# Optimization experiments

Hardware: AMD Instinct MI355X
Metric: run time of the kernel (lower is better)

## Reference

```python
import jax, jax.numpy as jnp
import numpy as np

# Constants from retinanet.settings (repo defaults, undefined in snippet; fixed here)
ALPHA = 0.95
GAMMA = 2.0
DAMPENING = 0.7           # DAMPENING_PARAMETER; gt_map simplified to all-False
MAX_POS_DIST = 30.0       # MAX_ANOT_ANCHOR_POSITION_DISTANCE
MAX_ANG_DIST = 20.0       # MAX_ANOT_ANCHOR_ANGLE_DISTANCE
EPS = 1e-4


def setup_inputs() -> dict:
    key = jax.random.key(0)
    k1, k2, k3, k4, k5 = jax.random.split(key, 5)
    B, N, K, C = 4, 300000, 64, 4
    classifications = jax.random.uniform(k1, (B, N, C), jnp.float32, 0.01, 0.99)
    regressions = jax.random.normal(k2, (B, N, 3), jnp.float32) * 5.0
    anchors = jax.random.uniform(k3, (B, N, 3), jnp.float32) * jnp.array([512.0, 512.0, 180.0])
    ann_xy_a = jax.random.uniform(k4, (B, K, 3), jnp.float32) * jnp.array([512.0, 512.0, 180.0])
    ann_cls = jax.random.randint(k5, (B, K, 1), 0, C).astype(jnp.float32)
    annotations = jnp.concatenate([ann_xy_a, ann_cls], axis=-1)  # [B,K,4]
    return {"classifications": classifications, "regressions": regressions,
            "anchors": anchors, "annotations": annotations}


def _per_image(classification, regression, ann, anchor):
    C = classification.shape[1]
    cls = jnp.clip(classification, EPS, 1.0 - EPS)
    # NxK broadcast distance matrices (the tile/transpose chain in the original)
    dx = jnp.abs(anchor[:, 0, None] - ann[None, :, 0])
    dy = jnp.abs(anchor[:, 1, None] - ann[None, :, 1])
    dalpha = jnp.abs(anchor[:, 2, None] - ann[None, :, 2])
    dxy = jnp.sqrt(dx * dx + dy * dy)                         # [N,K]
    dxy_min = jnp.min(dxy, axis=1)                            # [N]
    dxy_argmin = jnp.argmin(dxy, axis=1)                      # [N]
    a = jnp.take_along_axis(dalpha, dxy_argmin[:, None], axis=1)[:, 0]
    # target assignment
    neg = (dxy_min >= 1.5 * MAX_POS_DIST) | (a >= 1.5 * MAX_ANG_DIST)
    pos = (dxy_min < MAX_POS_DIST) & (a < MAX_ANG_DIST)
    assigned = ann[dxy_argmin]                                # [N,4] gather
    targets = jnp.full(cls.shape, -1.0, cls.dtype)
    targets = jnp.where(neg[:, None], 0.0, targets)
    targets = jnp.where(pos[:, None], 0.0, targets)
    onehot = jax.nn.one_hot(assigned[:, 3].astype(jnp.int32), C, dtype=cls.dtype)
    targets = jnp.where(pos[:, None] & (onehot > 0), 1.0, targets)
    num_pos = jnp.sum(pos).astype(cls.dtype)
    denom = jnp.maximum(num_pos, 1.0)
    # focal-weighted BCE
    alpha_factor = jnp.where(targets == 1.0, ALPHA, 1.0 - ALPHA)
    focal_weight = alpha_factor * jnp.where(targets == 1.0, 1.0 - cls, cls) ** GAMMA
    bce = -(targets * jnp.log(cls) + (1.0 - targets) * jnp.log(1.0 - cls))
    cls_loss = jnp.where(targets != -1.0, focal_weight * bce, 0.0) * DAMPENING
    cls_total = jnp.sum(cls_loss) / denom
    t = assigned[:, :3] - anchor
    diff_xy = jnp.abs(t[:, :2] - regression[:, :2])
    loss_xy = jnp.where(diff_xy <= 1.0 / 9.0, 0.5 * 9.0 * diff_xy ** 2, diff_xy - 0.5 / 9.0) * DAMPENING
    diff_ang = jnp.maximum((jnp.abs(t[:, 2] - regression[:, 2]) - 10.0) / 5.0, 0.0) * DAMPENING
    has_pos = num_pos > 0
    xy_mean = jnp.where(has_pos, jnp.sum(loss_xy * pos[:, None]) / (2.0 * denom), 0.0)
    ang_mean = jnp.where(has_pos, jnp.sum(diff_ang * pos) / denom, 0.0)
    return cls_total, xy_mean, ang_mean


def reference(classifications, regressions, anchors, annotations):
    anchor = anchors[0]  # original uses anchors[0,:,:] for all batch elements
    cls_l, xy_l, ang_l = jax.vmap(lambda c, r, an: _per_image(c, r, an, anchor))(
        classifications, regressions, annotations)
    return jnp.stack([jnp.mean(cls_l), jnp.mean(xy_l), jnp.mean(ang_l)])
```

## Files before the change

### kernel.cpp

```cpp
#include <hip/hip_runtime.h>
#include <cmath>

constexpr int Bk = 4;
constexpr int Nk = 300000;
constexpr int Kk = 64;
constexpr int BLOCK = 256;
constexpr int CHUNK = 4;
constexpr int SUPER = BLOCK * CHUNK;
constexpr int PBI = (Nk + SUPER - 1) / SUPER;
constexpr int NBLK = Bk * PBI;

#define C_ALPHA 0.95f
#define C_NALPHA (1.0f - 0.95f)
#define C_DAMP 0.7f


__global__ __launch_bounds__(BLOCK) void focal_main(
    const float* __restrict__ cls_,
    const float* __restrict__ reg_,
    const float* __restrict__ anc_,
    const float* __restrict__ ann_,
    float4* __restrict__ part)
{
    __shared__ float2 s_xy[Kk];
    __shared__ float  s_an[Kk];
    __shared__ float  s_cl[Kk];

    const int b   = blockIdx.x / PBI;
    const int blk = blockIdx.x - b * PBI;
    const int tid = threadIdx.x;
    const int a0  = blk * SUPER + tid * CHUNK;

    if (tid < Kk) {
        const float4 a4 = reinterpret_cast<const float4*>(ann_)[b * Kk + tid];
        s_xy[tid] = make_float2(a4.x, a4.y);
        s_an[tid] = a4.z;
        s_cl[tid] = a4.w;
    }
    __syncthreads();

    const bool full = (a0 + CHUNK) <= Nk;

    float ax[CHUNK], ay[CHUNK], aa[CHUNK];
    if (full) {
        const float4* a4p = reinterpret_cast<const float4*>(anc_);
        const int fb = 3 * (blk * BLOCK + tid);
        const float4 r0 = a4p[fb + 0];
        const float4 r1 = a4p[fb + 1];
        const float4 r2 = a4p[fb + 2];
        ax[0] = r0.x; ay[0] = r0.y; aa[0] = r0.z;
        ax[1] = r0.w; ay[1] = r1.x; aa[1] = r1.y;
        ax[2] = r1.z; ay[2] = r1.w; aa[2] = r2.x;
        ax[3] = r2.y; ay[3] = r2.z; aa[3] = r2.w;
    } else {
        #pragma unroll
        for (int c = 0; c < CHUNK; ++c) {
            const int n = a0 + c;
            if (n < Nk) {
                ax[c] = anc_[(size_t)n * 3 + 0];
                ay[c] = anc_[(size_t)n * 3 + 1];
                aa[c] = anc_[(size_t)n * 3 + 2];
            } else { ax[c] = 1e9f; ay[c] = 1e9f; aa[c] = 0.f; }
        }
    }

    float4 p4[CHUNK];
    if (full) {
        const float4* c4 = reinterpret_cast<const float4*>(cls_) + (size_t)b * Nk + a0;
        #pragma unroll
        for (int c = 0; c < CHUNK; ++c) p4[c] = c4[c];
    } else {
        #pragma unroll
        for (int c = 0; c < CHUNK; ++c) {
            const int n = a0 + c;
            p4[c] = (n < Nk) ? reinterpret_cast<const float4*>(cls_)[(size_t)b * Nk + n]
                             : make_float4(0.5f, 0.5f, 0.5f, 0.5f);
        }
    }

    float best[CHUNK];
    int   arg[CHUNK];
    #pragma unroll
    for (int c = 0; c < CHUNK; ++c) { best[c] = 3.4e38f; arg[c] = 0; }

    #pragma unroll
    for (int k = 0; k < Kk; ++k) {
        const float2 axy = s_xy[k];
        #pragma unroll
        for (int c = 0; c < CHUNK; ++c) {
            const float dx = ax[c] - axy.x;
            const float dy = ay[c] - axy.y;
            const float d  = fmaf(dy, dy, dx * dx);
            if (d < best[c]) { best[c] = d; arg[c] = k; }
        }
    }

    float cls_sum = 0.f, xy_sum = 0.f, ang_sum = 0.f, posn = 0.f;

    #pragma unroll
    for (int c = 0; c < CHUNK; ++c) {
        const bool  valid = full || (a0 + c < Nk);
        const int   a     = arg[c];
        const float aang  = fabsf(aa[c] - s_an[a]);
        const bool  posm  = valid && (best[c] < 900.0f)   && (aang < 20.0f);
        const bool  negm  = valid && ((best[c] >= 2025.0f) || (aang >= 30.0f));
        posn += posm ? 1.0f : 0.0f;

        const float p[4] = {p4[c].x, p4[c].y, p4[c].z, p4[c].w};
        float base = 0.f;
        #pragma unroll
        for (int cc = 0; cc < 4; ++cc) {
            const float pc = fminf(fmaxf(p[cc], 1e-4f), 1.0f - 1e-4f);
            base = fmaf(pc * pc, -__logf(1.0f - pc), base);
        }
        float s = C_NALPHA * base;
        if (posm) {
            const int cidx = (int)s_cl[a];
            float pc = (cidx < 2) ? (cidx == 0 ? p[0] : p[1])
                                  : (cidx == 2 ? p[2] : p[3]);
            pc = fminf(fmaxf(pc, 1e-4f), 1.0f - 1e-4f);
            s -= C_NALPHA * pc * pc * (-__logf(1.0f - pc));
            const float q = 1.0f - pc;
            s += C_ALPHA * q * q * (-__logf(pc));
        }
        cls_sum += (posm || negm) ? s * C_DAMP : 0.f;

        if (posm) {
            const size_t rb = ((size_t)b * Nk + (a0 + c)) * 3;
            const float rx = reg_[rb + 0];
            const float ry = reg_[rb + 1];
            const float ra = reg_[rb + 2];
            const float tx = s_xy[a].x - ax[c];
            const float ty = s_xy[a].y - ay[c];
            const float ta = s_an[a]   - aa[c];
            const float d0 = fabsf(tx - rx);
            const float d1 = fabsf(ty - ry);
            const float l0 = (d0 <= (1.0f / 9.0f)) ? 4.5f * d0 * d0 : d0 - (0.5f / 9.0f);
            const float l1 = (d1 <= (1.0f / 9.0f)) ? 4.5f * d1 * d1 : d1 - (0.5f / 9.0f);
            xy_sum += (l0 + l1) * C_DAMP;
            ang_sum += fmaxf((fabsf(ta - ra) - 10.0f) / 5.0f, 0.0f) * C_DAMP;
        }
    }

    #pragma unroll
    for (int off = 32; off > 0; off >>= 1) {
        cls_sum += __shfl_down(cls_sum, off, 64);
        xy_sum  += __shfl_down(xy_sum,  off, 64);
        ang_sum += __shfl_down(ang_sum, off, 64);
        posn    += __shfl_down(posn,    off, 64);
    }
    __shared__ float r0s[4], r1s[4], r2s[4], r3s[4];
    const int wave = tid >> 6;
    const int lane = tid & 63;
    if (lane == 0) { r0s[wave] = cls_sum; r1s[wave] = xy_sum; r2s[wave] = ang_sum; r3s[wave] = posn; }
    __syncthreads();
    if (tid == 0) {
        part[blockIdx.x] = make_float4(r0s[0] + r0s[1] + r0s[2] + r0s[3],
                                       r1s[0] + r1s[1] + r1s[2] + r1s[3],
                                       r2s[0] + r2s[1] + r2s[2] + r2s[3],
                                       r3s[0] + r3s[1] + r3s[2] + r3s[3]);
    }
}

__global__ __launch_bounds__(256) void focal_finalize(
    const float4* __restrict__ part, float* __restrict__ out)
{
    const int b    = threadIdx.x >> 6;
    const int lane = threadIdx.x & 63;
    double c = 0.0, x = 0.0, g = 0.0, q = 0.0;
    for (int i = lane; i < PBI; i += 64) {
        const float4 p = part[b * PBI + i];
        c += (double)p.x; x += (double)p.y; g += (double)p.z; q += (double)p.w;
    }
    #pragma unroll
    for (int off = 32; off > 0; off >>= 1) {
        c += __shfl_down(c, off, 64);
        x += __shfl_down(x, off, 64);
        g += __shfl_down(g, off, 64);
        q += __shfl_down(q, off, 64);
    }
    __shared__ double sc[4], sx[4], sg[4], sq[4];
    if (lane == 0) { sc[b] = c; sx[b] = x; sg[b] = g; sq[b] = q; }
    __syncthreads();
    if (threadIdx.x == 0) {
        double cm = 0.0, xm = 0.0, am = 0.0;
        for (int bb = 0; bb < Bk; ++bb) {
            const double np_   = sq[bb];
            const double denom = np_ > 1.0 ? np_ : 1.0;
            cm += sc[bb] / denom;
            if (np_ > 0.0) {
                xm += sx[bb] / (2.0 * denom);
                am += sg[bb] / denom;
            }
        }
        out[0] = (float)(cm / (double)Bk);
        out[1] = (float)(xm / (double)Bk);
        out[2] = (float)(am / (double)Bk);
    }
}

extern "C" void kernel_launch(void* const* d_in, const int* in_sizes, int n_in,
                              void* d_out, int out_size, void* d_ws, size_t ws_size,
                              hipStream_t stream)
{
    const float* cls_ = (const float*)d_in[0];
    const float* reg_ = (const float*)d_in[1];
    const float* anc_ = (const float*)d_in[2];
    const float* ann_ = (const float*)d_in[3];
    float4* part = (float4*)d_ws;

    focal_main<<<dim3(NBLK), dim3(BLOCK), 0, stream>>>(cls_, reg_, anc_, ann_, part);
    focal_finalize<<<dim3(1), dim3(256), 0, stream>>>(part, (float*)d_out);
}
```

Baseline: 102.2 us.

## Pack distance and index into uint min, use packed float math, prefetch regressions

The argmin over 64 annotations now packs the squared distance (low 6 mantissa bits cleared) with the annotation index into one unsigned integer and takes an integer min. This replaces the compare-and-select pair per candidate and lets the distance maths use packed two-wide float vectors. Regression values are now loaded unconditionally as coalesced float4 reads alongside the anchors, instead of as scattered scalar loads only for positive anchors. The trade-off is that truncating the distance can change which annotation wins a near tie and shifts the threshold comparisons slightly, and regression bytes are now read for every anchor.

```diff
diff --git a/kernel.cpp b/kernel.cpp
--- a/kernel.cpp
+++ b/kernel.cpp
@@ -1,5 +1,7 @@
 #include <hip/hip_runtime.h>
 #include <cmath>
+
+typedef float v2f __attribute__((ext_vector_type(2)));
 
 constexpr int Bk = 4;
 constexpr int Nk = 300000;
@@ -42,16 +44,29 @@
     const bool full = (a0 + CHUNK) <= Nk;
 
     float ax[CHUNK], ay[CHUNK], aa[CHUNK];
+    float rx[CHUNK], ry[CHUNK], ra[CHUNK];
+    float4 p4[CHUNK];
     if (full) {
         const float4* a4p = reinterpret_cast<const float4*>(anc_);
         const int fb = 3 * (blk * BLOCK + tid);
-        const float4 r0 = a4p[fb + 0];
-        const float4 r1 = a4p[fb + 1];
-        const float4 r2 = a4p[fb + 2];
-        ax[0] = r0.x; ay[0] = r0.y; aa[0] = r0.z;
-        ax[1] = r0.w; ay[1] = r1.x; aa[1] = r1.y;
-        ax[2] = r1.z; ay[2] = r1.w; aa[2] = r2.x;
-        ax[3] = r2.y; ay[3] = r2.z; aa[3] = r2.w;
+        const float4 A0 = a4p[fb + 0];
+        const float4 A1 = a4p[fb + 1];
+        const float4 A2 = a4p[fb + 2];
+        ax[0] = A0.x; ay[0] = A0.y; aa[0] = A0.z;
+        ax[1] = A0.w; ay[1] = A1.x; aa[1] = A1.y;
+        ax[2] = A1.z; ay[2] = A1.w; aa[2] = A2.x;
+        ax[3] = A2.y; ay[3] = A2.z; aa[3] = A2.w;
+        const float4* r4p = reinterpret_cast<const float4*>(reg_) + (size_t)b * (Nk * 3 / 4);
+        const float4 R0 = r4p[fb + 0];
+        const float4 R1 = r4p[fb + 1];
+        const float4 R2 = r4p[fb + 2];
+        rx[0] = R0.x; ry[0] = R0.y; ra[0] = R0.z;
+        rx[1] = R0.w; ry[1] = R1.x; ra[1] = R1.y;
+        rx[2] = R1.z; ry[2] = R1.w; ra[2] = R2.x;
+        rx[3] = R2.y; ry[3] = R2.z; ra[3] = R2.w;
+        const float4* c4 = reinterpret_cast<const float4*>(cls_) + (size_t)b * Nk + a0;
+        #pragma unroll
+        for (int c = 0; c < CHUNK; ++c) p4[c] = c4[c];
     } else {
         #pragma unroll
         for (int c = 0; c < CHUNK; ++c) {
@@ -60,38 +75,35 @@
                 ax[c] = anc_[(size_t)n * 3 + 0];
                 ay[c] = anc_[(size_t)n * 3 + 1];
                 aa[c] = anc_[(size_t)n * 3 + 2];
-            } else { ax[c] = 1e9f; ay[c] = 1e9f; aa[c] = 0.f; }
-        }
-    }
-
-    float4 p4[CHUNK];
-    if (full) {
-        const float4* c4 = reinterpret_cast<const float4*>(cls_) + (size_t)b * Nk + a0;
-        #pragma unroll
-        for (int c = 0; c < CHUNK; ++c) p4[c] = c4[c];
-    } else {
-        #pragma unroll
-        for (int c = 0; c < CHUNK; ++c) {
-            const int n = a0 + c;
-            p4[c] = (n < Nk) ? reinterpret_cast<const float4*>(cls_)[(size_t)b * Nk + n]
-                             : make_float4(0.5f, 0.5f, 0.5f, 0.5f);
-        }
-    }
-
-    float best[CHUNK];
-    int   arg[CHUNK];
-    #pragma unroll
-    for (int c = 0; c < CHUNK; ++c) { best[c] = 3.4e38f; arg[c] = 0; }
+                const size_t rb = ((size_t)b * Nk + n) * 3;
+                rx[c] = reg_[rb + 0]; ry[c] = reg_[rb + 1]; ra[c] = reg_[rb + 2];
+                p4[c] = reinterpret_cast<const float4*>(cls_)[(size_t)b * Nk + n];
+            } else {
+                ax[c] = 1e9f; ay[c] = 1e9f; aa[c] = 0.f;
+                rx[c] = 0.f; ry[c] = 0.f; ra[c] = 0.f;
+                p4[c] = make_float4(0.5f, 0.5f, 0.5f, 0.5f);
+            }
+        }
+    }
+
+    const v2f axp[2] = {{ax[0], ax[1]}, {ax[2], ax[3]}};
+    const v2f ayp[2] = {{ay[0], ay[1]}, {ay[2], ay[3]}};
+    unsigned int mn[CHUNK] = {0xFFFFFFFFu, 0xFFFFFFFFu, 0xFFFFFFFFu, 0xFFFFFFFFu};
 
     #pragma unroll
     for (int k = 0; k < Kk; ++k) {
         const float2 axy = s_xy[k];
-        #pragma unroll
-        for (int c = 0; c < CHUNK; ++c) {
-            const float dx = ax[c] - axy.x;
-            const float dy = ay[c] - axy.y;
-            const float d  = fmaf(dy, dy, dx * dx);
-            if (d < best[c]) { best[c] = d; arg[c] = k; }
+        const v2f kx = {axy.x, axy.x};
+        const v2f ky = {axy.y, axy.y};
+        #pragma unroll
+        for (int pp = 0; pp < 2; ++pp) {
+            const v2f dx = axp[pp] - kx;
+            const v2f dy = ayp[pp] - ky;
+            const v2f d  = dx * dx + dy * dy;
+            const unsigned int k0 = (__float_as_uint(d.x) & 0xFFFFFFC0u) | (unsigned int)k;
+            const unsigned int k1 = (__float_as_uint(d.y) & 0xFFFFFFC0u) | (unsigned int)k;
+            mn[2 * pp + 0] = min(mn[2 * pp + 0], k0);
+            mn[2 * pp + 1] = min(mn[2 * pp + 1], k1);
         }
     }
 
@@ -100,10 +112,11 @@
     #pragma unroll
     for (int c = 0; c < CHUNK; ++c) {
         const bool  valid = full || (a0 + c < Nk);
-        const int   a     = arg[c];
+        const int   a     = (int)(mn[c] & 63u);
+        const float bestq = __uint_as_float(mn[c] & 0xFFFFFFC0u);
         const float aang  = fabsf(aa[c] - s_an[a]);
-        const bool  posm  = valid && (best[c] < 900.0f)   && (aang < 20.0f);
-        const bool  negm  = valid && ((best[c] >= 2025.0f) || (aang >= 30.0f));
+        const bool  posm  = valid && (bestq < 900.0f)   && (aang < 20.0f);
+        const bool  negm  = valid && ((bestq >= 2025.0f) || (aang >= 30.0f));
         posn += posm ? 1.0f : 0.0f;
 
         const float p[4] = {p4[c].x, p4[c].y, p4[c].z, p4[c].w};
@@ -126,19 +139,15 @@
         cls_sum += (posm || negm) ? s * C_DAMP : 0.f;
 
         if (posm) {
-            const size_t rb = ((size_t)b * Nk + (a0 + c)) * 3;
-            const float rx = reg_[rb + 0];
-            const float ry = reg_[rb + 1];
-            const float ra = reg_[rb + 2];
             const float tx = s_xy[a].x - ax[c];
             const float ty = s_xy[a].y - ay[c];
             const float ta = s_an[a]   - aa[c];
-            const float d0 = fabsf(tx - rx);
-            const float d1 = fabsf(ty - ry);
+            const float d0 = fabsf(tx - rx[c]);
+            const float d1 = fabsf(ty - ry[c]);
             const float l0 = (d0 <= (1.0f / 9.0f)) ? 4.5f * d0 * d0 : d0 - (0.5f / 9.0f);
             const float l1 = (d1 <= (1.0f / 9.0f)) ? 4.5f * d1 * d1 : d1 - (0.5f / 9.0f);
             xy_sum += (l0 + l1) * C_DAMP;
-            ang_sum += fmaxf((fabsf(ta - ra) - 10.0f) / 5.0f, 0.0f) * C_DAMP;
+            ang_sum += fmaxf((fabsf(ta - ra[c]) - 10.0f) / 5.0f, 0.0f) * C_DAMP;
         }
     }
 
```

Result: slower. 113.4 us (+10.9%).

## Pack distance and index into one uint key for argmin, read annotations from global

Applied to the files above, without the earlier changes.

Replaces the compare-and-select argmin with a single unsigned min over a key that packs the squared distance (low 6 mantissa bits cleared) with the annotation index. The inner loop now reads annotations straight from global memory through uniform loads, and the shared-memory fill is moved so its barrier overlaps with the distance loop. A launch-bounds occupancy hint is also added. Truncating the distance mantissa can flip near-ties and threshold comparisons, which slightly changes the results.

```diff
diff --git a/kernel.cpp b/kernel.cpp
--- a/kernel.cpp
+++ b/kernel.cpp
@@ -15,29 +15,22 @@
 #define C_DAMP 0.7f
 
 
-__global__ __launch_bounds__(BLOCK) void focal_main(
+__global__ __launch_bounds__(BLOCK, 6) void focal_main(
     const float* __restrict__ cls_,
     const float* __restrict__ reg_,
     const float* __restrict__ anc_,
     const float* __restrict__ ann_,
     float4* __restrict__ part)
 {
-    __shared__ float2 s_xy[Kk];
-    __shared__ float  s_an[Kk];
-    __shared__ float  s_cl[Kk];
+    __shared__ float4 s_ann[Kk];
 
     const int b   = blockIdx.x / PBI;
     const int blk = blockIdx.x - b * PBI;
     const int tid = threadIdx.x;
     const int a0  = blk * SUPER + tid * CHUNK;
 
-    if (tid < Kk) {
-        const float4 a4 = reinterpret_cast<const float4*>(ann_)[b * Kk + tid];
-        s_xy[tid] = make_float2(a4.x, a4.y);
-        s_an[tid] = a4.z;
-        s_cl[tid] = a4.w;
-    }
-    __syncthreads();
+    if (tid < Kk)
+        s_ann[tid] = reinterpret_cast<const float4*>(ann_)[b * Kk + tid];
 
     const bool full = (a0 + CHUNK) <= Nk;
 
@@ -45,13 +38,13 @@
     if (full) {
         const float4* a4p = reinterpret_cast<const float4*>(anc_);
         const int fb = 3 * (blk * BLOCK + tid);
-        const float4 r0 = a4p[fb + 0];
-        const float4 r1 = a4p[fb + 1];
-        const float4 r2 = a4p[fb + 2];
-        ax[0] = r0.x; ay[0] = r0.y; aa[0] = r0.z;
-        ax[1] = r0.w; ay[1] = r1.x; aa[1] = r1.y;
-        ax[2] = r1.z; ay[2] = r1.w; aa[2] = r2.x;
-        ax[3] = r2.y; ay[3] = r2.z; aa[3] = r2.w;
+        const float4 A0 = a4p[fb + 0];
+        const float4 A1 = a4p[fb + 1];
+        const float4 A2 = a4p[fb + 2];
+        ax[0] = A0.x; ay[0] = A0.y; aa[0] = A0.z;
+        ax[1] = A0.w; ay[1] = A1.x; aa[1] = A1.y;
+        ax[2] = A1.z; ay[2] = A1.w; aa[2] = A2.x;
+        ax[3] = A2.y; ay[3] = A2.z; aa[3] = A2.w;
     } else {
         #pragma unroll
         for (int c = 0; c < CHUNK; ++c) {
@@ -64,6 +57,24 @@
         }
     }
 
+    const float4* __restrict__ annb = reinterpret_cast<const float4*>(ann_) + b * Kk;
+    unsigned int mn[CHUNK] = {0xFFFFFFFFu, 0xFFFFFFFFu, 0xFFFFFFFFu, 0xFFFFFFFFu};
+
+    #pragma unroll
+    for (int k = 0; k < Kk; ++k) {
+        const float4 A = annb[k];
+        #pragma unroll
+        for (int c = 0; c < CHUNK; ++c) {
+            const float dx = ax[c] - A.x;
+            const float dy = ay[c] - A.y;
+            const float d  = fmaf(dy, dy, dx * dx);
+            const unsigned int key = (__float_as_uint(d) & 0xFFFFFFC0u) | (unsigned int)k;
+            mn[c] = min(mn[c], key);
+        }
+    }
+
+    __syncthreads();
+
     float4 p4[CHUNK];
     if (full) {
         const float4* c4 = reinterpret_cast<const float4*>(cls_) + (size_t)b * Nk + a0;
@@ -78,32 +89,17 @@
         }
     }
 
-    float best[CHUNK];
-    int   arg[CHUNK];
-    #pragma unroll
-    for (int c = 0; c < CHUNK; ++c) { best[c] = 3.4e38f; arg[c] = 0; }
-
-    #pragma unroll
-    for (int k = 0; k < Kk; ++k) {
-        const float2 axy = s_xy[k];
-        #pragma unroll
-        for (int c = 0; c < CHUNK; ++c) {
-            const float dx = ax[c] - axy.x;
-            const float dy = ay[c] - axy.y;
-            const float d  = fmaf(dy, dy, dx * dx);
-            if (d < best[c]) { best[c] = d; arg[c] = k; }
-        }
-    }
-
     float cls_sum = 0.f, xy_sum = 0.f, ang_sum = 0.f, posn = 0.f;
 
     #pragma unroll
     for (int c = 0; c < CHUNK; ++c) {
         const bool  valid = full || (a0 + c < Nk);
-        const int   a     = arg[c];
-        const float aang  = fabsf(aa[c] - s_an[a]);
-        const bool  posm  = valid && (best[c] < 900.0f)   && (aang < 20.0f);
-        const bool  negm  = valid && ((best[c] >= 2025.0f) || (aang >= 30.0f));
+        const int   a     = (int)(mn[c] & 63u);
+        const float bestq = __uint_as_float(mn[c] & 0xFFFFFFC0u);
+        const float4 An   = s_ann[a];
+        const float aang  = fabsf(aa[c] - An.z);
+        const bool  posm  = valid && (bestq < 900.0f)   && (aang < 20.0f);
+        const bool  negm  = valid && ((bestq >= 2025.0f) || (aang >= 30.0f));
         posn += posm ? 1.0f : 0.0f;
 
         const float p[4] = {p4[c].x, p4[c].y, p4[c].z, p4[c].w};
@@ -115,7 +111,7 @@
         }
         float s = C_NALPHA * base;
         if (posm) {
-            const int cidx = (int)s_cl[a];
+            const int cidx = (int)An.w;
             float pc = (cidx < 2) ? (cidx == 0 ? p[0] : p[1])
                                   : (cidx == 2 ? p[2] : p[3]);
             pc = fminf(fmaxf(pc, 1e-4f), 1.0f - 1e-4f);
@@ -130,9 +126,9 @@
             const float rx = reg_[rb + 0];
             const float ry = reg_[rb + 1];
             const float ra = reg_[rb + 2];
-            const float tx = s_xy[a].x - ax[c];
-            const float ty = s_xy[a].y - ay[c];
-            const float ta = s_an[a]   - aa[c];
+            const float tx = An.x - ax[c];
+            const float ty = An.y - ay[c];
+            const float ta = An.z - aa[c];
             const float d0 = fabsf(tx - rx);
             const float d1 = fabsf(ty - ry);
             const float l0 = (d0 <= (1.0f / 9.0f)) ? 4.5f * d0 * d0 : d0 - (0.5f / 9.0f);
```

Measured after the change: 99.85 us. 1.02x faster.
